# Performance work log

Hardware: AMD Instinct MI355X
Metric: run time of the kernel (lower is better)

Reference implementation:

```python
import jax, jax.numpy as jnp
import numpy as np

N_HEADS = 4
D_K = 64
SCALE = D_K ** -0.5


def setup_inputs() -> dict:
    key = jax.random.key(0)
    k1, k2, k3 = jax.random.split(key, 3)
    B, C, S = 8, 256, 2048
    x = jax.random.normal(k1, (B, C, S), dtype=jnp.float32)
    # Linear(C, 3*H*dk): weight [out, in] as in torch
    w_proj = jax.random.normal(k2, (3 * N_HEADS * D_K, C), dtype=jnp.float32) * (C ** -0.5)
    b_proj = jnp.zeros((3 * N_HEADS * D_K,), dtype=jnp.float32)
    w_out = jax.random.normal(k3, (C, N_HEADS * D_K), dtype=jnp.float32) * ((N_HEADS * D_K) ** -0.5)
    b_out = jnp.zeros((C,), dtype=jnp.float32)
    return {"x": x, "w_proj": w_proj, "b_proj": b_proj, "w_out": w_out, "b_out": b_out}


def reference(x, w_proj, b_proj, w_out, b_out):
    B, C, S = x.shape
    xt = jnp.transpose(x, (0, 2, 1))                    # [B, S, C]
    qkv = xt @ w_proj.T + b_proj                        # [B, S, 3*H*dk]
    qkv = qkv.reshape(B, S, N_HEADS, 3 * D_K)
    q, k, v = jnp.split(qkv, 3, axis=-1)                # each [B, S, H, dk]
    attn = jnp.einsum('bihd,bjhd->bijh', q, k) * SCALE  # [B, S, S, H]
    attn = jax.nn.softmax(attn, axis=2)                 # softmax over key axis j
    res = jnp.einsum('bijh,bjhd->bihd', attn, v)        # [B, S, H, dk]
    res = res.reshape(B, S, N_HEADS * D_K)
    res = res @ w_out.T + b_out + xt                    # residual in [B, S, C]
    return jnp.transpose(res, (0, 2, 1))                # back to [B, C, S]
```

## Files before the change

kernel.cpp:

```cpp
#include <hip/hip_runtime.h>


typedef _Float16 f16;
typedef __attribute__((ext_vector_type(4))) float f32x4;
typedef __attribute__((ext_vector_type(8))) _Float16 h8;
typedef __attribute__((ext_vector_type(4))) _Float16 h4;
typedef __attribute__((ext_vector_type(2))) __fp16 fp16x2;
typedef __attribute__((ext_vector_type(4))) __fp16 fp16x4;
typedef __attribute__((ext_vector_type(8))) __fp16 fp16x8;

#define SS 2048
#define CC 256
#define BB 8
#define HH 4
#define DK 64
#define O3 768
#define NT64 32
#define C1F 0.1803368801111204f
#define C2L2 11.541560327111707f

#define MFMA32(a, b, c) __builtin_amdgcn_mfma_f32_16x16x32_f16(a, b, c, 0, 0, 0)

#if __has_builtin(__builtin_amdgcn_exp2f)
#define EXP2(x) __builtin_amdgcn_exp2f(x)
#else
#define EXP2(x) exp2f(x)
#endif

__device__ __forceinline__ void async_ld16(const f16* g, f16* lds) {
  __builtin_amdgcn_global_load_lds(
      (const __attribute__((address_space(1))) unsigned int*)g,
      (__attribute__((address_space(3))) unsigned int*)lds, 16, 0, 0);
}

__global__ __launch_bounds__(256) void k_prep(const float* __restrict__ x,
                                              f16* __restrict__ xt,
                                              const float* __restrict__ w_proj,
                                              const float* __restrict__ w_out,
                                              f16* __restrict__ wp, f16* __restrict__ wo) {
  if (blockIdx.z == 8) {
    int slice = blockIdx.y * 32 + blockIdx.x;
    int i0 = slice * 2048 + threadIdx.x * 8;
    const float* src;
    f16* dst;
    if (i0 < O3 * CC) {
      src = w_proj + i0;
      int row = i0 >> 8, ch = (i0 & 255) >> 3;
      dst = wp + row * 256 + ((ch ^ (row & 7)) << 3);
    } else {
      int j = i0 - O3 * CC;
      src = w_out + j;
      int row = j >> 8, ch = (j & 255) >> 3;
      dst = wo + row * 256 + ((ch ^ (row & 7)) << 3);
    }
    float4 a = *(const float4*)src;
    float4 b = *(const float4*)(src + 4);
    h8 v = {(f16)a.x, (f16)a.y, (f16)a.z, (f16)a.w,
            (f16)b.x, (f16)b.y, (f16)b.z, (f16)b.w};
    *(h8*)dst = v;
    return;
  }
  __shared__ float tile[64][65];
  int b = blockIdx.z, c0 = blockIdx.y * 64, s0 = blockIdx.x * 64;
  int t = threadIdx.x;
#pragma unroll
  for (int it = 0; it < 16; ++it) {
    int idx = it * 256 + t;
    int cl = idx >> 6, sl = idx & 63;
    tile[cl][sl] = x[(size_t)(b * CC + c0 + cl) * SS + s0 + sl];
  }
  __syncthreads();
#pragma unroll
  for (int cid = t; cid < 512; cid += 256) {
    int sl = cid >> 3, chl = cid & 7;
    int s = s0 + sl;
    int gch = (c0 >> 3) + chl;
    h8 v;
#pragma unroll
    for (int e = 0; e < 8; ++e) v[e] = (f16)tile[chl * 8 + e][sl];
    *(h8*)(xt + (size_t)(b * SS + s) * CC + ((gch ^ (s & 7)) << 3)) = v;
  }
}

__global__ __launch_bounds__(256) void k_qkv(const f16* __restrict__ xt,
                                             const f16* __restrict__ wp,
                                             const float* __restrict__ bp,
                                             f16* __restrict__ qh, f16* __restrict__ ksw,
                                             f16* __restrict__ vsw) {
  __shared__ f16 As[16384];
  __shared__ f16 Bs[16384];
  __shared__ f16 Ot[4096];
  int b = blockIdx.z;
  int oti = blockIdx.y, o0 = oti * 64;
  int s0 = blockIdx.x * 64;
  int w = threadIdx.x >> 6, l = threadIdx.x & 63;
  int lr = l & 15, lg = l >> 4;

  const f16* Ag = xt + ((size_t)b * SS + s0) * CC;
  const f16* Bg = wp + (size_t)o0 * CC;
#pragma unroll
  for (int i = 0; i < 8; ++i) {
    int off = w * 4096 + i * 512;
    async_ld16(Ag + off + l * 8, &As[off]);
    async_ld16(Bg + off + l * 8, &Bs[off]);
  }
  asm volatile("s_waitcnt vmcnt(0)" ::: "memory");
  __syncthreads();

  f32x4 acc[4] = {};
#pragma unroll
  for (int kk = 0; kk < CC; kk += 32) {
    int chs = (((kk >> 3) + lg) ^ (lr & 7)) << 3;
    h8 af = *(const h8*)&As[(w * 16 + lr) * 256 + chs];
#pragma unroll
    for (int n = 0; n < 4; ++n) {
      h8 bf = *(const h8*)&Bs[(n * 16 + lr) * 256 + chs];
      acc[n] = MFMA32(af, bf, acc[n]);
    }
  }

  int seg = oti % 3;
  int h = oti / 3;
  int bh = b * HH + h;
  float scl = (seg == 0) ? C1F : 1.0f;
#pragma unroll
  for (int n = 0; n < 4; ++n) {
    float bb = bp[o0 + n * 16 + lr];
#pragma unroll
    for (int r = 0; r < 4; ++r) acc[n][r] = (acc[n][r] + bb) * scl;
  }

  if (seg == 2) {
#pragma unroll
    for (int n = 0; n < 4; ++n) {
      int d = n * 16 + lr;
#pragma unroll
      for (int r = 0; r < 4; ++r) {
        int sl = w * 16 + lg * 4 + r;
        int kl = sl & 31;
        int ps = ((kl & 15) >> 2) ^ ((d >> 1) & 3);
        Ot[(sl >> 5) * 2048 + d * 32 + ps * 8 + ((kl >> 4) << 2) + (kl & 3)] =
            (f16)acc[n][r];
      }
    }
  } else if (seg == 1) {
#pragma unroll
    for (int n = 0; n < 4; ++n) {
      int d = n * 16 + lr;
#pragma unroll
      for (int r = 0; r < 4; ++r) {
        int sl = w * 16 + lg * 4 + r;
        int kl = sl & 31;
        Ot[(sl >> 5) * 2048 + kl * 64 + (((d >> 3) ^ (kl & 7)) << 3) + (d & 7)] =
            (f16)acc[n][r];
      }
    }
  } else {
#pragma unroll
    for (int n = 0; n < 4; ++n)
#pragma unroll
      for (int r = 0; r < 4; ++r)
        Ot[(w * 16 + lg * 4 + r) * 64 + n * 16 + lr] = (f16)acc[n][r];
  }
  __syncthreads();

  int t = threadIdx.x;
  f16* dst;
  if (seg == 0)
    dst = qh + ((size_t)bh * SS + s0) * DK;
  else if (seg == 1)
    dst = ksw + ((size_t)bh * NT64 + (s0 >> 6)) * 4096;
  else
    dst = vsw + ((size_t)bh * NT64 + (s0 >> 6)) * 4096;
  *(int4*)(dst + t * 16) = *(const int4*)&Ot[t * 16];
  *(int4*)(dst + t * 16 + 8) = *(const int4*)&Ot[t * 16 + 8];
}

__global__ __launch_bounds__(256, 4) void k_attn(const f16* __restrict__ qh,
                                                 const f16* __restrict__ ksw,
                                                 const f16* __restrict__ vsw,
                                                 f16* __restrict__ res) {
  __shared__ f16 kbuf[2][4096];
  __shared__ f16 vbuf[2][4096];
  int id = blockIdx.x;
  int xcd = id & 7, slot = id >> 3;
  int bh = xcd * 4 + (slot >> 5);
  int qt = slot & 31;
  int w = threadIdx.x >> 6, l = threadIdx.x & 63;
  int qg = w & 1, kg = w >> 1;
  int q0w = qt * 64 + qg * 32;
  int lr = l & 15, lg = l >> 4;

  h8 qf[2][2];
#pragma unroll
  for (int qs = 0; qs < 2; ++qs) {
    const f16* qp = qh + (size_t)(bh * SS + q0w + qs * 16 + lr) * DK;
    qf[qs][0] = *(const h8*)(qp + lg * 8);
    qf[qs][1] = *(const h8*)(qp + 32 + lg * 8);
  }

  const f16* kg_ = ksw + (size_t)bh * (SS * DK);
  const f16* vg_ = vsw + (size_t)bh * (SS * DK);

#define STAGE(bufi, tile)                                            \
  {                                                                  \
    const f16* kq = kg_ + (size_t)(tile) * 4096 + w * 1024 + l * 8;  \
    const f16* vq = vg_ + (size_t)(tile) * 4096 + w * 1024 + l * 8;  \
    f16* kd = &kbuf[bufi][w * 1024];                                 \
    f16* vd = &vbuf[bufi][w * 1024];                                 \
    async_ld16(kq, kd);                                              \
    async_ld16(kq + 512, kd + 512);                                  \
    async_ld16(vq, vd);                                              \
    async_ld16(vq + 512, vd + 512);                                  \
  }

  int swk = (lr & 7) << 3;
  int ek[2][2];
#pragma unroll
  for (int kb = 0; kb < 2; ++kb)
#pragma unroll
    for (int ch = 0; ch < 2; ++ch)
      ek[kb][ch] = (lr + kb * 16) * 64 + ((ch * 32 + lg * 8) ^ swk);
  int ev = lr * 32 + ((lg ^ ((lr >> 1) & 3)) * 8);

  f32x4 oacc[2][4] = {};
  f32x4 dacc[2] = {};
  const f32x4 cinit = {-C2L2, -C2L2, -C2L2, -C2L2};
  const h8 ones8 = {(f16)1.0f, (f16)1.0f, (f16)1.0f, (f16)1.0f,
                    (f16)1.0f, (f16)1.0f, (f16)1.0f, (f16)1.0f};

  int sb = kg * 2048;

  STAGE(0, 0);
  STAGE(1, 1);

  for (int kt = 0; kt < NT64; ++kt) {
    int cur = kt & 1;
    asm volatile("s_waitcnt vmcnt(4)" ::: "memory");
    __builtin_amdgcn_sched_barrier(0);
    __builtin_amdgcn_s_barrier();
    __builtin_amdgcn_sched_barrier(0);

    const f16* kb_ = &kbuf[cur][sb];
    const f16* vb_ = &vbuf[cur][sb];
    h8 kf[2][2];
#pragma unroll
    for (int kb = 0; kb < 2; ++kb)
#pragma unroll
      for (int ch = 0; ch < 2; ++ch) kf[kb][ch] = *(const h8*)&kb_[ek[kb][ch]];
    h8 vv[4];
#pragma unroll
    for (int m = 0; m < 4; ++m) vv[m] = *(const h8*)&vb_[ev + m * 512];

    __builtin_amdgcn_s_setprio(1);
    f32x4 sacc[2][2];
#pragma unroll
    for (int qs = 0; qs < 2; ++qs)
#pragma unroll
      for (int kb = 0; kb < 2; ++kb) {
        sacc[qs][kb] = MFMA32(kf[kb][0], qf[qs][0], cinit);
        sacc[qs][kb] = MFMA32(kf[kb][1], qf[qs][1], sacc[qs][kb]);
      }
    h8 pf8[2];
#pragma unroll
    for (int qs = 0; qs < 2; ++qs) {
      float e0 = EXP2(sacc[qs][0][0]);
      float e1 = EXP2(sacc[qs][0][1]);
      float e2 = EXP2(sacc[qs][0][2]);
      float e3 = EXP2(sacc[qs][0][3]);
      float e4 = EXP2(sacc[qs][1][0]);
      float e5 = EXP2(sacc[qs][1][1]);
      float e6 = EXP2(sacc[qs][1][2]);
      float e7 = EXP2(sacc[qs][1][3]);
      fp16x2 p01 = __builtin_amdgcn_cvt_pkrtz(e0, e1);
      fp16x2 p23 = __builtin_amdgcn_cvt_pkrtz(e2, e3);
      fp16x2 p45 = __builtin_amdgcn_cvt_pkrtz(e4, e5);
      fp16x2 p67 = __builtin_amdgcn_cvt_pkrtz(e6, e7);
      fp16x4 lo4 = __builtin_shufflevector(p01, p23, 0, 1, 2, 3);
      fp16x4 hi4 = __builtin_shufflevector(p45, p67, 0, 1, 2, 3);
      fp16x8 p8 = __builtin_shufflevector(lo4, hi4, 0, 1, 2, 3, 4, 5, 6, 7);
      pf8[qs] = __builtin_bit_cast(h8, p8);
    }
#pragma unroll
    for (int qs = 0; qs < 2; ++qs) dacc[qs] = MFMA32(ones8, pf8[qs], dacc[qs]);
#pragma unroll
    for (int qs = 0; qs < 2; ++qs)
#pragma unroll
      for (int m = 0; m < 4; ++m) oacc[qs][m] = MFMA32(vv[m], pf8[qs], oacc[qs][m]);
    __builtin_amdgcn_s_setprio(0);

    __builtin_amdgcn_sched_barrier(0);
    __builtin_amdgcn_s_barrier();
    __builtin_amdgcn_sched_barrier(0);
    int nxt = (kt + 2) & (NT64 - 1);
    STAGE(cur, nxt);
  }

  asm volatile("s_waitcnt vmcnt(0)" ::: "memory");
  __syncthreads();

  float* red = (float*)&kbuf[0][0];
  float* redd = (float*)&vbuf[0][0];
  if (kg == 1) {
#pragma unroll
    for (int qs = 0; qs < 2; ++qs) {
#pragma unroll
      for (int m = 0; m < 4; ++m)
        *(f32x4*)&red[(qg * 8 + qs * 4 + m) * 256 + l * 4] = oacc[qs][m];
      redd[(qg * 2 + qs) * 64 + l] = dacc[qs][0];
    }
  }
  __syncthreads();
  if (kg == 0) {
    int b = bh >> 2, h = bh & 3;
#pragma unroll
    for (int qs = 0; qs < 2; ++qs) {
      float inv = 1.0f / (dacc[qs][0] + redd[(qg * 2 + qs) * 64 + l]);
      int s = q0w + qs * 16 + lr;
      f16* rrow = res + (size_t)(b * SS + s) * CC;
      int sk = s & 7;
#pragma unroll
      for (int m = 0; m < 4; ++m) {
        f32x4 o2 = *(const f32x4*)&red[(qg * 8 + qs * 4 + m) * 256 + l * 4];
        int d = h * 64 + m * 16 + lg * 4;
        int ch = d >> 3;
        h4 rv;
#pragma unroll
        for (int r = 0; r < 4; ++r) rv[r] = (f16)((oacc[qs][m][r] + o2[r]) * inv);
        *(h4*)(rrow + ((ch ^ sk) << 3) + (d & 7)) = rv;
      }
    }
  }
}

__global__ __launch_bounds__(256) void k_out(const f16* __restrict__ res,
                                             const f16* __restrict__ wo,
                                             const float* __restrict__ bo,
                                             const float* __restrict__ x,
                                             float* __restrict__ out) {
  __shared__ f16 As[16384];
  __shared__ f16 Bs[16384];
  __shared__ float Xs[4096];
  float* Ot = (float*)As;

  int b = blockIdx.z;
  int c0 = blockIdx.y * 64;
  int s0 = blockIdx.x * 64;
  int w = threadIdx.x >> 6, l = threadIdx.x & 63;
  int lr = l & 15, lg = l >> 4;

  const f16* Ag = res + ((size_t)b * SS + s0) * CC;
  const f16* Bg = wo + (size_t)c0 * CC;
#pragma unroll
  for (int i = 0; i < 8; ++i) {
    int off = w * 4096 + i * 512;
    async_ld16(Ag + off + l * 8, &As[off]);
    async_ld16(Bg + off + l * 8, &Bs[off]);
  }
#pragma unroll
  for (int i = 0; i < 4; ++i) {
    int cl = w * 16 + i * 4 + (l >> 4);
    int cidx = l & 15;
    const float* src =
        x + ((size_t)b * CC + c0 + cl) * SS + s0 + ((cidx ^ (cl & 7)) << 2);
    async_ld16((const f16*)src, (f16*)&Xs[w * 1024 + i * 256 + l * 4]);
  }
  asm volatile("s_waitcnt vmcnt(0)" ::: "memory");
  __syncthreads();

  f32x4 acc[4] = {};
#pragma unroll
  for (int kk = 0; kk < CC; kk += 32) {
    int chs = (((kk >> 3) + lg) ^ (lr & 7)) << 3;
    h8 af = *(const h8*)&As[(w * 16 + lr) * 256 + chs];
#pragma unroll
    for (int n = 0; n < 4; ++n) {
      h8 bf = *(const h8*)&Bs[(n * 16 + lr) * 256 + chs];
      acc[n] = MFMA32(af, bf, acc[n]);
    }
  }
  __syncthreads();

#pragma unroll
  for (int n = 0; n < 4; ++n) {
    int c = c0 + n * 16 + lr;
    float bb = bo[c];
    float4 xv =
        *(const float4*)&Xs[(n * 16 + lr) * 64 + (((w * 4 + lg) ^ (lr & 7)) << 2)];
    float4 ov;
    ov.x = acc[n][0] + bb + xv.x;
    ov.y = acc[n][1] + bb + xv.y;
    ov.z = acc[n][2] + bb + xv.z;
    ov.w = acc[n][3] + bb + xv.w;
    *(float4*)&Ot[(n * 16 + lr) * 68 + w * 16 + lg * 4] = ov;
  }
  __syncthreads();

  int cl = threadIdx.x >> 2, sc = (threadIdx.x & 3) * 16;
  float* orow = out + ((size_t)b * CC + c0 + cl) * SS + s0 + sc;
  const float* srow = &Ot[cl * 68 + sc];
#pragma unroll
  for (int j = 0; j < 4; ++j) *(float4*)(orow + j * 4) = *(const float4*)(srow + j * 4);
}

extern "C" void kernel_launch(void* const* d_in, const int* in_sizes, int n_in,
                              void* d_out, int out_size, void* d_ws, size_t ws_size,
                              hipStream_t stream) {
  const float* x = (const float*)d_in[0];
  const float* w_proj = (const float*)d_in[1];
  const float* b_proj = (const float*)d_in[2];
  const float* w_out = (const float*)d_in[3];
  const float* b_out = (const float*)d_in[4];
  float* out = (float*)d_out;

  char* p = (char*)d_ws;
  f16* xt = (f16*)p; p += (size_t)BB * SS * CC * 2;
  f16* wp = (f16*)p; p += (size_t)O3 * CC * 2;
  f16* wo = (f16*)p; p += (size_t)CC * CC * 2;
  f16* qh = (f16*)p; p += (size_t)BB * HH * SS * DK * 2;
  f16* ksw = (f16*)p; p += (size_t)BB * HH * SS * DK * 2;
  f16* vsw = (f16*)p; p += (size_t)BB * HH * SS * DK * 2;
  f16* res = (f16*)p;

  k_prep<<<dim3(SS / 64, CC / 64, BB + 1), 256, 0, stream>>>(x, xt, w_proj, w_out, wp, wo);
  k_qkv<<<dim3(SS / 64, O3 / 64, BB), 256, 0, stream>>>(xt, wp, b_proj, qh, ksw, vsw);
  k_attn<<<dim3(1024), 256, 0, stream>>>(qh, ksw, vsw, res);
  k_out<<<dim3(SS / 64, CC / 64, BB), 256, 0, stream>>>(res, wo, b_out, x, out);
}
```

Measured before the change: 85.87 us.

## Double query rows per attention block and replace ones-MFMA row sum with scalar adds

Each attention block now handles 128 query rows (64 per wave) instead of 64, halving the grid to 512 blocks. Every K/V tile staged in shared memory is therefore reused across twice as many queries, halving K/V traffic per query. The softmax denominator is now accumulated with VALU adds plus cross-lane shuffles instead of an extra MFMA against a ones vector. The cost is more registers (occupancy hint lowered from 4 to 3), a two-pass reduction epilogue with extra barriers, and fewer blocks to spread across CUs.

```diff
diff --git a/kernel.cpp b/kernel.cpp
--- a/kernel.cpp
+++ b/kernel.cpp
@@ -176,7 +176,7 @@
   *(int4*)(dst + t * 16 + 8) = *(const int4*)&Ot[t * 16 + 8];
 }
 
-__global__ __launch_bounds__(256, 4) void k_attn(const f16* __restrict__ qh,
+__global__ __launch_bounds__(256, 3) void k_attn(const f16* __restrict__ qh,
                                                  const f16* __restrict__ ksw,
                                                  const f16* __restrict__ vsw,
                                                  f16* __restrict__ res) {
@@ -184,16 +184,16 @@
   __shared__ f16 vbuf[2][4096];
   int id = blockIdx.x;
   int xcd = id & 7, slot = id >> 3;
-  int bh = xcd * 4 + (slot >> 5);
-  int qt = slot & 31;
+  int bh = xcd * 4 + (slot >> 4);
+  int qt = slot & 15;
   int w = threadIdx.x >> 6, l = threadIdx.x & 63;
   int qg = w & 1, kg = w >> 1;
-  int q0w = qt * 64 + qg * 32;
+  int q0w = qt * 128 + qg * 64;
   int lr = l & 15, lg = l >> 4;
 
-  h8 qf[2][2];
-#pragma unroll
-  for (int qs = 0; qs < 2; ++qs) {
+  h8 qf[4][2];
+#pragma unroll
+  for (int qs = 0; qs < 4; ++qs) {
     const f16* qp = qh + (size_t)(bh * SS + q0w + qs * 16 + lr) * DK;
     qf[qs][0] = *(const h8*)(qp + lg * 8);
     qf[qs][1] = *(const h8*)(qp + 32 + lg * 8);
@@ -223,11 +223,9 @@
       ek[kb][ch] = (lr + kb * 16) * 64 + ((ch * 32 + lg * 8) ^ swk);
   int ev = lr * 32 + ((lg ^ ((lr >> 1) & 3)) * 8);
 
-  f32x4 oacc[2][4] = {};
-  f32x4 dacc[2] = {};
+  f32x4 oacc[4][4] = {};
+  float dsum[4] = {0.f, 0.f, 0.f, 0.f};
   const f32x4 cinit = {-C2L2, -C2L2, -C2L2, -C2L2};
-  const h8 ones8 = {(f16)1.0f, (f16)1.0f, (f16)1.0f, (f16)1.0f,
-                    (f16)1.0f, (f16)1.0f, (f16)1.0f, (f16)1.0f};
 
   int sb = kg * 2048;
 
@@ -253,25 +251,23 @@
     for (int m = 0; m < 4; ++m) vv[m] = *(const h8*)&vb_[ev + m * 512];
 
     __builtin_amdgcn_s_setprio(1);
-    f32x4 sacc[2][2];
-#pragma unroll
-    for (int qs = 0; qs < 2; ++qs)
+#pragma unroll
+    for (int qs = 0; qs < 4; ++qs) {
+      f32x4 sacc[2];
 #pragma unroll
       for (int kb = 0; kb < 2; ++kb) {
-        sacc[qs][kb] = MFMA32(kf[kb][0], qf[qs][0], cinit);
-        sacc[qs][kb] = MFMA32(kf[kb][1], qf[qs][1], sacc[qs][kb]);
+        sacc[kb] = MFMA32(kf[kb][0], qf[qs][0], cinit);
+        sacc[kb] = MFMA32(kf[kb][1], qf[qs][1], sacc[kb]);
       }
-    h8 pf8[2];
-#pragma unroll
-    for (int qs = 0; qs < 2; ++qs) {
-      float e0 = EXP2(sacc[qs][0][0]);
-      float e1 = EXP2(sacc[qs][0][1]);
-      float e2 = EXP2(sacc[qs][0][2]);
-      float e3 = EXP2(sacc[qs][0][3]);
-      float e4 = EXP2(sacc[qs][1][0]);
-      float e5 = EXP2(sacc[qs][1][1]);
-      float e6 = EXP2(sacc[qs][1][2]);
-      float e7 = EXP2(sacc[qs][1][3]);
+      float e0 = EXP2(sacc[0][0]);
+      float e1 = EXP2(sacc[0][1]);
+      float e2 = EXP2(sacc[0][2]);
+      float e3 = EXP2(sacc[0][3]);
+      float e4 = EXP2(sacc[1][0]);
+      float e5 = EXP2(sacc[1][1]);
+      float e6 = EXP2(sacc[1][2]);
+      float e7 = EXP2(sacc[1][3]);
+      dsum[qs] += ((e0 + e1) + (e2 + e3)) + ((e4 + e5) + (e6 + e7));
       fp16x2 p01 = __builtin_amdgcn_cvt_pkrtz(e0, e1);
       fp16x2 p23 = __builtin_amdgcn_cvt_pkrtz(e2, e3);
       fp16x2 p45 = __builtin_amdgcn_cvt_pkrtz(e4, e5);
@@ -279,14 +275,10 @@
       fp16x4 lo4 = __builtin_shufflevector(p01, p23, 0, 1, 2, 3);
       fp16x4 hi4 = __builtin_shufflevector(p45, p67, 0, 1, 2, 3);
       fp16x8 p8 = __builtin_shufflevector(lo4, hi4, 0, 1, 2, 3, 4, 5, 6, 7);
-      pf8[qs] = __builtin_bit_cast(h8, p8);
-    }
-#pragma unroll
-    for (int qs = 0; qs < 2; ++qs) dacc[qs] = MFMA32(ones8, pf8[qs], dacc[qs]);
-#pragma unroll
-    for (int qs = 0; qs < 2; ++qs)
-#pragma unroll
-      for (int m = 0; m < 4; ++m) oacc[qs][m] = MFMA32(vv[m], pf8[qs], oacc[qs][m]);
+      h8 pf8 = __builtin_bit_cast(h8, p8);
+#pragma unroll
+      for (int m = 0; m < 4; ++m) oacc[qs][m] = MFMA32(vv[m], pf8, oacc[qs][m]);
+    }
     __builtin_amdgcn_s_setprio(0);
 
     __builtin_amdgcn_sched_barrier(0);
@@ -296,6 +288,12 @@
     STAGE(cur, nxt);
   }
 
+#pragma unroll
+  for (int qs = 0; qs < 4; ++qs) {
+    dsum[qs] += __shfl_xor(dsum[qs], 16, 64);
+    dsum[qs] += __shfl_xor(dsum[qs], 32, 64);
+  }
+
   asm volatile("s_waitcnt vmcnt(0)" ::: "memory");
   __syncthreads();
 
@@ -303,33 +301,41 @@
   float* redd = (float*)&vbuf[0][0];
   if (kg == 1) {
 #pragma unroll
-    for (int qs = 0; qs < 2; ++qs) {
-#pragma unroll
-      for (int m = 0; m < 4; ++m)
-        *(f32x4*)&red[(qg * 8 + qs * 4 + m) * 256 + l * 4] = oacc[qs][m];
-      redd[(qg * 2 + qs) * 64 + l] = dacc[qs][0];
-    }
-  }
-  __syncthreads();
-  if (kg == 0) {
-    int b = bh >> 2, h = bh & 3;
-#pragma unroll
-    for (int qs = 0; qs < 2; ++qs) {
-      float inv = 1.0f / (dacc[qs][0] + redd[(qg * 2 + qs) * 64 + l]);
-      int s = q0w + qs * 16 + lr;
-      f16* rrow = res + (size_t)(b * SS + s) * CC;
-      int sk = s & 7;
-#pragma unroll
-      for (int m = 0; m < 4; ++m) {
-        f32x4 o2 = *(const f32x4*)&red[(qg * 8 + qs * 4 + m) * 256 + l * 4];
-        int d = h * 64 + m * 16 + lg * 4;
-        int ch = d >> 3;
-        h4 rv;
-#pragma unroll
-        for (int r = 0; r < 4; ++r) rv[r] = (f16)((oacc[qs][m][r] + o2[r]) * inv);
-        *(h4*)(rrow + ((ch ^ sk) << 3) + (d & 7)) = rv;
+    for (int qs = 0; qs < 4; ++qs) redd[(qg * 4 + qs) * 64 + l] = dsum[qs];
+  }
+  int b = bh >> 2, h = bh & 3;
+#pragma unroll
+  for (int half = 0; half < 2; ++half) {
+    if (kg == 1) {
+#pragma unroll
+      for (int q2 = 0; q2 < 2; ++q2)
+#pragma unroll
+        for (int m = 0; m < 4; ++m)
+          *(f32x4*)&red[((qg * 2 + q2) * 4 + m) * 256 + l * 4] =
+              oacc[half * 2 + q2][m];
+    }
+    __syncthreads();
+    if (kg == 0) {
+#pragma unroll
+      for (int q2 = 0; q2 < 2; ++q2) {
+        int qs = half * 2 + q2;
+        float inv = 1.0f / (dsum[qs] + redd[(qg * 4 + qs) * 64 + l]);
+        int s = q0w + qs * 16 + lr;
+        f16* rrow = res + (size_t)(b * SS + s) * CC;
+        int sk = s & 7;
+#pragma unroll
+        for (int m = 0; m < 4; ++m) {
+          f32x4 o2 = *(const f32x4*)&red[((qg * 2 + q2) * 4 + m) * 256 + l * 4];
+          int d = h * 64 + m * 16 + lg * 4;
+          int ch = d >> 3;
+          h4 rv;
+#pragma unroll
+          for (int r = 0; r < 4; ++r) rv[r] = (f16)((oacc[qs][m][r] + o2[r]) * inv);
+          *(h4*)(rrow + ((ch ^ sk) << 3) + (d & 7)) = rv;
+        }
       }
     }
+    __syncthreads();
   }
 }
 
@@ -424,6 +430,6 @@
 
   k_prep<<<dim3(SS / 64, CC / 64, BB + 1), 256, 0, stream>>>(x, xt, w_proj, w_out, wp, wo);
   k_qkv<<<dim3(SS / 64, O3 / 64, BB), 256, 0, stream>>>(xt, wp, b_proj, qh, ksw, vsw);
-  k_attn<<<dim3(1024), 256, 0, stream>>>(qh, ksw, vsw, res);
+  k_attn<<<dim3(512), 256, 0, stream>>>(qh, ksw, vsw, res);
   k_out<<<dim3(SS / 64, CC / 64, BB), 256, 0, stream>>>(res, wo, b_out, x, out);
 }
```

Measured after the change: 86.84 us. About the same (+1.1%).

## Replace MFMA-based softmax denominator with VALU sums and remap GEMM block indices

Applied to the files above, without the earlier changes.

In the attention kernel, the row-sum of exponentials is now accumulated as scalar fp32 adds per lane and reduced across lane groups with shuffles at the end, replacing the extra MFMA against a ones vector each tile. The QKV and output projection kernels switch from 3D grids to a flat 1D grid whose index puts the batch in the low bits, so consecutive workgroups span batches and share weight tiles, which may change L2 and XCD locality. The sum now uses unrounded fp32 exponentials rather than the fp16-rounded ones fed to the PV product, which slightly changes normalization numerics. It adds VALU work to the exp section while removing MFMA issue slots.

```diff
diff --git a/kernel.cpp b/kernel.cpp
--- a/kernel.cpp
+++ b/kernel.cpp
@@ -90,9 +90,11 @@
   __shared__ f16 As[16384];
   __shared__ f16 Bs[16384];
   __shared__ f16 Ot[4096];
-  int b = blockIdx.z;
-  int oti = blockIdx.y, o0 = oti * 64;
-  int s0 = blockIdx.x * 64;
+  int id = blockIdx.x;
+  int b = id & 7;
+  int rest = id >> 3;
+  int oti = rest % 12, o0 = oti * 64;
+  int s0 = (rest / 12) * 64;
   int w = threadIdx.x >> 6, l = threadIdx.x & 63;
   int lr = l & 15, lg = l >> 4;
 
@@ -224,10 +226,8 @@
   int ev = lr * 32 + ((lg ^ ((lr >> 1) & 3)) * 8);
 
   f32x4 oacc[2][4] = {};
-  f32x4 dacc[2] = {};
+  float dsum[2] = {0.f, 0.f};
   const f32x4 cinit = {-C2L2, -C2L2, -C2L2, -C2L2};
-  const h8 ones8 = {(f16)1.0f, (f16)1.0f, (f16)1.0f, (f16)1.0f,
-                    (f16)1.0f, (f16)1.0f, (f16)1.0f, (f16)1.0f};
 
   int sb = kg * 2048;
 
@@ -272,6 +272,7 @@
       float e5 = EXP2(sacc[qs][1][1]);
       float e6 = EXP2(sacc[qs][1][2]);
       float e7 = EXP2(sacc[qs][1][3]);
+      dsum[qs] += ((e0 + e1) + (e2 + e3)) + ((e4 + e5) + (e6 + e7));
       fp16x2 p01 = __builtin_amdgcn_cvt_pkrtz(e0, e1);
       fp16x2 p23 = __builtin_amdgcn_cvt_pkrtz(e2, e3);
       fp16x2 p45 = __builtin_amdgcn_cvt_pkrtz(e4, e5);
@@ -282,8 +283,6 @@
       pf8[qs] = __builtin_bit_cast(h8, p8);
     }
 #pragma unroll
-    for (int qs = 0; qs < 2; ++qs) dacc[qs] = MFMA32(ones8, pf8[qs], dacc[qs]);
-#pragma unroll
     for (int qs = 0; qs < 2; ++qs)
 #pragma unroll
       for (int m = 0; m < 4; ++m) oacc[qs][m] = MFMA32(vv[m], pf8[qs], oacc[qs][m]);
@@ -296,6 +295,12 @@
     STAGE(cur, nxt);
   }
 
+#pragma unroll
+  for (int qs = 0; qs < 2; ++qs) {
+    dsum[qs] += __shfl_xor(dsum[qs], 16, 64);
+    dsum[qs] += __shfl_xor(dsum[qs], 32, 64);
+  }
+
   asm volatile("s_waitcnt vmcnt(0)" ::: "memory");
   __syncthreads();
 
@@ -307,7 +312,7 @@
 #pragma unroll
       for (int m = 0; m < 4; ++m)
         *(f32x4*)&red[(qg * 8 + qs * 4 + m) * 256 + l * 4] = oacc[qs][m];
-      redd[(qg * 2 + qs) * 64 + l] = dacc[qs][0];
+      redd[(qg * 2 + qs) * 64 + l] = dsum[qs];
     }
   }
   __syncthreads();
@@ -315,7 +320,7 @@
     int b = bh >> 2, h = bh & 3;
 #pragma unroll
     for (int qs = 0; qs < 2; ++qs) {
-      float inv = 1.0f / (dacc[qs][0] + redd[(qg * 2 + qs) * 64 + l]);
+      float inv = 1.0f / (dsum[qs] + redd[(qg * 2 + qs) * 64 + l]);
       int s = q0w + qs * 16 + lr;
       f16* rrow = res + (size_t)(b * SS + s) * CC;
       int sk = s & 7;
@@ -343,9 +348,11 @@
   __shared__ float Xs[4096];
   float* Ot = (float*)As;
 
-  int b = blockIdx.z;
-  int c0 = blockIdx.y * 64;
-  int s0 = blockIdx.x * 64;
+  int id = blockIdx.x;
+  int b = id & 7;
+  int rest = id >> 3;
+  int c0 = (rest & 3) * 64;
+  int s0 = (rest >> 2) * 64;
   int w = threadIdx.x >> 6, l = threadIdx.x & 63;
   int lr = l & 15, lg = l >> 4;
 
@@ -423,7 +430,7 @@
   f16* res = (f16*)p;
 
   k_prep<<<dim3(SS / 64, CC / 64, BB + 1), 256, 0, stream>>>(x, xt, w_proj, w_out, wp, wo);
-  k_qkv<<<dim3(SS / 64, O3 / 64, BB), 256, 0, stream>>>(xt, wp, b_proj, qh, ksw, vsw);
+  k_qkv<<<dim3(3072), 256, 0, stream>>>(xt, wp, b_proj, qh, ksw, vsw);
   k_attn<<<dim3(1024), 256, 0, stream>>>(qh, ksw, vsw, res);
-  k_out<<<dim3(SS / 64, CC / 64, BB), 256, 0, stream>>>(res, wo, b_out, x, out);
-}
+  k_out<<<dim3(1024), 256, 0, stream>>>(res, wo, b_out, x, out);
+}
```

After: 89.54 us. 4.3% more time.
